# Performance work log

Hardware: AMD Instinct MI355X
Metric: run time of the kernel (lower is better)

The kernel has to match this reference:

```python
import jax, jax.numpy as jnp
import numpy as np

EMBED_DIM = 768
NUM_HEADS = 12
HEAD_DIM = EMBED_DIM // NUM_HEADS
B, N = 16, 512


def setup_inputs() -> dict:
    key = jax.random.key(0)
    ks = jax.random.split(key, 13)
    s = 1.0 / np.sqrt(EMBED_DIM)
    return {
        "query": jax.random.normal(ks[0], (B, N, EMBED_DIM), jnp.float32),
        "key_in": jax.random.normal(ks[1], (B, N, EMBED_DIM), jnp.float32),
        "value": jax.random.normal(ks[2], (B, N, EMBED_DIM), jnp.float32),
        "spatial_bias": jax.random.normal(ks[3], (B, N, N), jnp.float32),
        "edge_bias": jax.random.normal(ks[4], (B, N, N), jnp.float32),
        "Wq": jax.random.uniform(ks[5], (EMBED_DIM, EMBED_DIM), jnp.float32, -s, s),
        "bq": jax.random.uniform(ks[6], (EMBED_DIM,), jnp.float32, -s, s),
        "Wk": jax.random.uniform(ks[7], (EMBED_DIM, EMBED_DIM), jnp.float32, -s, s),
        "bk": jax.random.uniform(ks[8], (EMBED_DIM,), jnp.float32, -s, s),
        "Wv": jax.random.uniform(ks[9], (EMBED_DIM, EMBED_DIM), jnp.float32, -s, s),
        "bv": jax.random.uniform(ks[10], (EMBED_DIM,), jnp.float32, -s, s),
        "Wo": jax.random.uniform(ks[11], (EMBED_DIM, EMBED_DIM), jnp.float32, -s, s),
        "bo": jax.random.uniform(ks[12], (EMBED_DIM,), jnp.float32, -s, s),
    }


def reference(query, key_in, value, spatial_bias, edge_bias,
              Wq, bq, Wk, bk, Wv, bv, Wo, bo):
    b, n, e = query.shape
    h, d = NUM_HEADS, HEAD_DIM
    scale = d ** -0.5
    # projections (torch Linear: x @ W.T + b), reshape to [b, h, n, d]
    Q = (query @ Wq.T + bq).reshape(b, n, h, d).transpose(0, 2, 1, 3)
    K = (key_in @ Wk.T + bk).reshape(b, n, h, d).transpose(0, 2, 1, 3)
    V = (value @ Wv.T + bv).reshape(b, n, h, d).transpose(0, 2, 1, 3)
    # scores: [b, h, n, n] with additive spatial + edge bias broadcast over heads
    scores = jnp.einsum('bhnd,bhmd->bhnm', Q, K) * scale
    scores = scores + spatial_bias[:, None, :, :] + edge_bias[:, None, :, :]
    attn_weights = jax.nn.softmax(scores, axis=-1)
    attn_output = jnp.einsum('bhnm,bhmd->bhnd', attn_weights, V)
    attn_output = attn_output.transpose(0, 2, 1, 3).reshape(b, n, e)
    attn_output = attn_output @ Wo.T + bo
    return attn_output, attn_weights
```

## Files before the change

kernel.cpp:

```cpp
#include <hip/hip_runtime.h>

using bf16x8 = __attribute__((ext_vector_type(8))) __bf16;
using f32x4  = __attribute__((ext_vector_type(4))) float;
using u16 = unsigned short;

constexpr int Bb = 16, Nn = 512, Ee = 768, Hh = 12, Dd = 64;

__device__ inline u16 f2b(float x) {
  union { float f; unsigned int u; } v; v.f = x;
  unsigned int r = v.u + 0x7fffu + ((v.u >> 16) & 1u);
  return (u16)(r >> 16);
}

__device__ inline unsigned cvtpk(float lo, float hi) {
  unsigned r;
  asm("v_cvt_pk_bf16_f32 %0, %1, %2" : "=v"(r) : "v"(lo), "v"(hi));
  return r;
}

__device__ inline void gload16(const void* g, void* l) {
  __builtin_amdgcn_global_load_lds((const __attribute__((address_space(1))) void*)g,
                                   (__attribute__((address_space(3))) void*)l, 16, 0, 0);
}

#define MFMA __builtin_amdgcn_mfma_f32_16x16x32_bf16

__global__ void k_cvt(const float* __restrict__ w0, const float* __restrict__ w1,
                      const float* __restrict__ w2, const float* __restrict__ w3,
                      u16* __restrict__ dstW,
                      const float* __restrict__ sb, const float* __restrict__ eb,
                      u16* __restrict__ cb) {
  int idx = blockIdx.x * 256 + threadIdx.x;
  constexpr int perW = Ee * Ee / 4;
  constexpr int totW = 4 * perW;
  if (idx < totW) {
    int m = idx / perW, r = idx - m * perW;
    const float* src = (m == 0) ? w0 : (m == 1) ? w1 : (m == 2) ? w2 : w3;
    float4 v = reinterpret_cast<const float4*>(src)[r];
    ushort4 o = make_ushort4(f2b(v.x), f2b(v.y), f2b(v.z), f2b(v.w));
    reinterpret_cast<ushort4*>(dstW)[idx] = o;
  } else {
    int k = idx - totW;
    float4 s0 = reinterpret_cast<const float4*>(sb)[k * 2];
    float4 s1 = reinterpret_cast<const float4*>(sb)[k * 2 + 1];
    float4 e0 = reinterpret_cast<const float4*>(eb)[k * 2];
    float4 e1 = reinterpret_cast<const float4*>(eb)[k * 2 + 1];
    ushort4 o0 = make_ushort4(f2b(s0.x + e0.x), f2b(s0.y + e0.y), f2b(s0.z + e0.z), f2b(s0.w + e0.w));
    ushort4 o1 = make_ushort4(f2b(s1.x + e1.x), f2b(s1.y + e1.y), f2b(s1.z + e1.z), f2b(s1.w + e1.w));
    reinterpret_cast<ushort4*>(cb)[k * 2] = o0;
    reinterpret_cast<ushort4*>(cb)[k * 2 + 1] = o1;
  }
}

__global__ __launch_bounds__(256, 3)
void k_qkv(const float* __restrict__ xq, const float* __restrict__ xk, const float* __restrict__ xv,
           const u16* __restrict__ wb, const float* __restrict__ bq, const float* __restrict__ bk,
           const float* __restrict__ bv, u16* __restrict__ Q, u16* __restrict__ K,
           u16* __restrict__ VT) {
  const int mat = blockIdx.z;
  const float* X = (mat == 0) ? xq : (mat == 1) ? xk : xv;
  const u16* W = wb + (size_t)mat * Ee * Ee;
  const float* bias = (mat == 0) ? bq : (mat == 1) ? bk : bv;
  const int bm = blockIdx.x, bn = blockIdx.y;
  const int tid = threadIdx.x, lane = tid & 63, wid = tid >> 6;
  const int wr = wid >> 1, wc = wid & 1;

  __shared__ char smem[49152];

  auto stageA = [&](int buf, int it) {
    const int r0 = tid >> 3, s = tid & 7;
    char* lbase = smem + buf * 16384 + tid * 16;
#pragma unroll
    for (int R = 0; R < 4; ++R) {
      const int row = R * 32 + r0;
      const int ch = s ^ (row & 7);
      gload16(X + (size_t)(bm * 128 + row) * Ee + it * 32 + ch * 4, lbase + R * 4096);
    }
  };
  auto stageB = [&](int buf, int it) {
    const int r0 = tid >> 2, s = tid & 3;
    char* lbase = smem + 32768 + buf * 8192 + tid * 16;
#pragma unroll
    for (int R = 0; R < 2; ++R) {
      const int row = R * 64 + r0;
      const int ch = s ^ ((row >> 1) & 3);
      gload16(W + (size_t)(bn * 128 + row) * Ee + it * 32 + ch * 8, lbase + R * 4096);
    }
  };

  f32x4 acc[4][4] = {};

  auto compute = [&](int buf) {
    const char* Ab = smem + buf * 16384;
    const char* Bbp = smem + 32768 + buf * 8192;
    const int q = lane >> 4;
    bf16x8 a[4], b[4];
#pragma unroll
    for (int mt = 0; mt < 4; ++mt) {
      const int row = wr * 64 + mt * 16 + (lane & 15);
      const int s0 = (2 * q) ^ (row & 7), s1 = (2 * q + 1) ^ (row & 7);
      f32x4 f0 = *reinterpret_cast<const f32x4*>(Ab + row * 128 + s0 * 16);
      f32x4 f1 = *reinterpret_cast<const f32x4*>(Ab + row * 128 + s1 * 16);
      union { unsigned u[4]; bf16x8 v; } cv;
      cv.u[0] = cvtpk(f0[0], f0[1]);
      cv.u[1] = cvtpk(f0[2], f0[3]);
      cv.u[2] = cvtpk(f1[0], f1[1]);
      cv.u[3] = cvtpk(f1[2], f1[3]);
      a[mt] = cv.v;
    }
#pragma unroll
    for (int nt = 0; nt < 4; ++nt) {
      const int row = wc * 64 + nt * 16 + (lane & 15);
      const int s = q ^ ((row >> 1) & 3);
      b[nt] = *reinterpret_cast<const bf16x8*>(Bbp + row * 64 + s * 16);
    }
#pragma unroll
    for (int mt = 0; mt < 4; ++mt)
#pragma unroll
      for (int nt = 0; nt < 4; ++nt)
        acc[mt][nt] = MFMA(a[mt], b[nt], acc[mt][nt], 0, 0, 0);
  };

  stageA(0, 0); stageB(0, 0);
  __syncthreads();
  int buf = 0;
  for (int it = 0; it < 24; ++it) {
    if (it + 1 < 24) { stageA(buf ^ 1, it + 1); stageB(buf ^ 1, it + 1); }
    compute(buf);
    __syncthreads();
    buf ^= 1;
  }

  u16* sm16 = (u16*)smem;
  if (mat < 2) {
    u16* dst = (mat == 0) ? Q : K;
    const float sc = (mat == 0) ? 0.125f : 1.0f;
#pragma unroll
    for (int mt = 0; mt < 4; ++mt) {
      const int n_l0 = wr * 64 + mt * 16 + ((lane >> 4) << 2);
#pragma unroll
      for (int nt = 0; nt < 4; ++nt) {
        const int e_l = wc * 64 + nt * 16 + (lane & 15);
        const float bs = bias[bn * 128 + e_l];
#pragma unroll
        for (int j = 0; j < 4; ++j)
          sm16[(n_l0 + j) * 136 + e_l] = f2b((acc[mt][nt][j] + bs) * sc);
      }
    }
    __syncthreads();
    const int row = tid >> 1, half = tid & 1;
    const int n = bm * 128 + row, b = n >> 9, n0 = n & 511, h = bn * 2 + half;
    u16* gp = dst + ((size_t)(b * Hh + h) * Nn + n0) * Dd;
    const u16* sp = sm16 + row * 136 + half * 64;
#pragma unroll
    for (int i = 0; i < 8; ++i)
      *reinterpret_cast<int4*>(gp + i * 8) = *reinterpret_cast<const int4*>(sp + i * 8);
  } else {
#pragma unroll
    for (int mt = 0; mt < 4; ++mt) {
      const int n_l0 = wr * 64 + mt * 16 + ((lane >> 4) << 2);
#pragma unroll
      for (int nt = 0; nt < 4; ++nt) {
        const int e_l = wc * 64 + nt * 16 + (lane & 15);
        const float bs = bias[bn * 128 + e_l];
#pragma unroll
        for (int j = 0; j < 4; ++j)
          sm16[e_l * 136 + n_l0 + j] = f2b(acc[mt][nt][j] + bs);
      }
    }
    __syncthreads();
    const int er = tid >> 1, half = tid & 1;
    const int b = bm >> 2, h = bn * 2 + (er >> 6), d = er & 63;
    u16* gp = VT + ((size_t)(b * Hh + h) * Dd + d) * Nn + (bm & 3) * 128 + half * 64;
    const u16* sp = sm16 + er * 136 + half * 64;
#pragma unroll
    for (int i = 0; i < 8; ++i)
      *reinterpret_cast<int4*>(gp + i * 8) = *reinterpret_cast<const int4*>(sp + i * 8);
  }
}

__global__ __launch_bounds__(256, 2)
void k_attn(const u16* __restrict__ Q, const u16* __restrict__ K,
            const u16* __restrict__ cb, const u16* __restrict__ VT,
            float* __restrict__ wout, u16* __restrict__ AO) {
  const int flat = blockIdx.x + 8 * (blockIdx.y + Hh * blockIdx.z);
  const int c = flat & 7, j = flat >> 3;
  const int g = c + 8 * (j % 24);
  const int qb = j / 24;
  const int h = g % Hh, b = g / Hh;
  const int bh = b * Hh + h;
  const int q0 = qb * 64;
  const int tid = threadIdx.x, lane = tid & 63, wid = tid >> 6;
  const int l15 = lane & 15, q4 = lane >> 4;

  __shared__ char smem[65536];

  bf16x8 aq[2];
  {
    const u16* qp = Q + ((size_t)bh * Nn + q0 + wid * 16 + l15) * Dd + q4 * 8;
    aq[0] = *reinterpret_cast<const bf16x8*>(qp);
    aq[1] = *reinterpret_cast<const bf16x8*>(qp + 32);
  }

  const int rql = wid * 16 + l15;
  const int rq = q0 + rql;
  const u16* cbp = cb + ((size_t)b * Nn + rq) * Nn + q4 * 4;
  uint2 cbr[32];
#pragma unroll
  for (int t = 0; t < 32; ++t)
    cbr[t] = *reinterpret_cast<const uint2*>(cbp + t * 16);

#pragma unroll
  for (int i = 0; i < 16; ++i) {
    const int s = i * 256 + tid;
    const int row = s >> 3, cs = s & 7;
    gload16(K + ((size_t)bh * Nn + row) * Dd + (cs ^ (row & 7)) * 8, smem + s * 16);
  }
  __syncthreads();

  f32x4 acc[32] = {};
  __builtin_amdgcn_s_setprio(1);
#pragma unroll
  for (int kt = 0; kt < 8; ++kt)
#pragma unroll
    for (int kk = 0; kk < 2; ++kk)
#pragma unroll
      for (int ct = 0; ct < 4; ++ct) {
        const int r = kt * 64 + ct * 16 + l15;
        bf16x8 bk = *reinterpret_cast<const bf16x8*>(
            smem + r * 128 + (((kk * 4 + q4) ^ (r & 7)) * 16));
        acc[kt * 4 + ct] = MFMA(bk, aq[kk], acc[kt * 4 + ct], 0, 0, 0);
      }
  __builtin_amdgcn_s_setprio(0);

#pragma unroll
  for (int t = 0; t < 32; ++t) {
    acc[t][0] += __uint_as_float((unsigned)cbr[t].x << 16);
    acc[t][1] += __uint_as_float(cbr[t].x & 0xffff0000u);
    acc[t][2] += __uint_as_float((unsigned)cbr[t].y << 16);
    acc[t][3] += __uint_as_float(cbr[t].y & 0xffff0000u);
  }

  float mx = -1e30f;
#pragma unroll
  for (int t = 0; t < 32; ++t)
#pragma unroll
    for (int j2 = 0; j2 < 4; ++j2) mx = fmaxf(mx, acc[t][j2]);
  mx = fmaxf(mx, __shfl_xor(mx, 16));
  mx = fmaxf(mx, __shfl_xor(mx, 32));

  float sum = 0.f;
#pragma unroll
  for (int t = 0; t < 32; ++t)
#pragma unroll
    for (int j2 = 0; j2 < 4; ++j2) {
      float p = exp2f((acc[t][j2] - mx) * 1.44269504f);
      acc[t][j2] = p;
      sum += p;
    }
  sum += __shfl_xor(sum, 16);
  sum += __shfl_xor(sum, 32);
  const float inv = 1.0f / sum;

  __syncthreads();

  const u16* Vb = VT + ((size_t)bh * Dd + l15) * Nn + q4 * 8;
  bf16x8 vb0[8], vb1[8];
  auto loadV = [&](int kt, bf16x8* d) {
#pragma unroll
    for (int kk = 0; kk < 2; ++kk)
#pragma unroll
      for (int ct = 0; ct < 4; ++ct)
        d[kk * 4 + ct] = *reinterpret_cast<const bf16x8*>(
            Vb + (size_t)(ct * 16) * Nn + kt * 64 + kk * 32);
  };
  loadV(0, vb0);
  loadV(1, vb1);

  char* Pb = smem + rql * 1024;
#pragma unroll
  for (int t = 0; t < 32; ++t) {
    uint2 pk;
    pk.x = cvtpk(acc[t][0] * inv, acc[t][1] * inv);
    pk.y = cvtpk(acc[t][2] * inv, acc[t][3] * inv);
    const int chunk = (2 * t + (q4 >> 1)) ^ (rql & 7);
    *reinterpret_cast<uint2*>(Pb + chunk * 16 + (q4 & 1) * 8) = pk;
  }
  __syncthreads();

  f32x4 acc2[4] = {};
  const int qr = rql;
  const char* Pr = smem + qr * 1024;
  f32x4* wp4 = reinterpret_cast<f32x4*>(wout + ((size_t)bh * Nn + rq) * Nn);
  auto storeW = [&](int kt) {
#pragma unroll
    for (int u = 0; u < 4; ++u) {
      const int t = kt * 4 + u;
      f32x4 o;
      o[0] = acc[t][0] * inv; o[1] = acc[t][1] * inv;
      o[2] = acc[t][2] * inv; o[3] = acc[t][3] * inv;
      __builtin_nontemporal_store(o, &wp4[t * 4 + q4]);
    }
  };
#pragma unroll
  for (int kp = 0; kp < 4; ++kp) {
    const int ktA = 2 * kp, ktB = 2 * kp + 1;
    __builtin_amdgcn_s_setprio(1);
#pragma unroll
    for (int kk = 0; kk < 2; ++kk) {
      const int chunk = (ktA * 8 + kk * 4 + q4) ^ (qr & 7);
      bf16x8 pa = *reinterpret_cast<const bf16x8*>(Pr + chunk * 16);
#pragma unroll
      for (int ct = 0; ct < 4; ++ct)
        acc2[ct] = MFMA(pa, vb0[kk * 4 + ct], acc2[ct], 0, 0, 0);
    }
    __builtin_amdgcn_s_setprio(0);
    if (ktA + 2 < 8) loadV(ktA + 2, vb0);
    storeW(ktA);
    __builtin_amdgcn_s_setprio(1);
#pragma unroll
    for (int kk = 0; kk < 2; ++kk) {
      const int chunk = (ktB * 8 + kk * 4 + q4) ^ (qr & 7);
      bf16x8 pa = *reinterpret_cast<const bf16x8*>(Pr + chunk * 16);
#pragma unroll
      for (int ct = 0; ct < 4; ++ct)
        acc2[ct] = MFMA(pa, vb1[kk * 4 + ct], acc2[ct], 0, 0, 0);
    }
    __builtin_amdgcn_s_setprio(0);
    if (ktB + 2 < 8) loadV(ktB + 2, vb1);
    storeW(ktB);
  }

  __syncthreads();
  u16* ao_t = (u16*)smem;
#pragma unroll
  for (int ct = 0; ct < 4; ++ct)
#pragma unroll
    for (int j2 = 0; j2 < 4; ++j2)
      ao_t[(wid * 16 + q4 * 4 + j2) * 72 + ct * 16 + l15] = f2b(acc2[ct][j2]);
  __syncthreads();
  {
    const int row = tid >> 3, ch = tid & 7;
#pragma unroll
    for (int i = 0; i < 2; ++i) {
      const int r = row + i * 32;
      int4 v = *reinterpret_cast<const int4*>(ao_t + r * 72 + ch * 8);
      *reinterpret_cast<int4*>(AO + ((size_t)b * Nn + q0 + r) * Ee + h * Dd + ch * 8) = v;
    }
  }
}

__global__ __launch_bounds__(256, 4)
void k_outproj(const u16* __restrict__ AOp, const u16* __restrict__ Wo,
               const float* __restrict__ bo, float* __restrict__ out) {
  const int bm = blockIdx.x, bn = blockIdx.y;
  const int tid = threadIdx.x, lane = tid & 63, wid = tid >> 6;
  const int wr = wid >> 1, wc = wid & 1;

  __shared__ char smem[32768];

  auto stage = [&](const u16* src, int lds_base, int buf, int it) {
    const int r0 = tid >> 2, s = tid & 3;
    char* lbase = smem + lds_base + buf * 8192 + tid * 16;
#pragma unroll
    for (int R = 0; R < 2; ++R) {
      const int row = R * 64 + r0;
      const int ch = s ^ ((row >> 1) & 3);
      gload16(src + (size_t)row * Ee + it * 32 + ch * 8, lbase + R * 4096);
    }
  };

  f32x4 acc[4][4] = {};

  auto compute = [&](int buf) {
    const char* Ab = smem + buf * 8192;
    const char* Bbp = smem + 16384 + buf * 8192;
    const int q = lane >> 4;
    bf16x8 a[4], b[4];
#pragma unroll
    for (int mt = 0; mt < 4; ++mt) {
      const int row = wr * 64 + mt * 16 + (lane & 15);
      const int s = q ^ ((row >> 1) & 3);
      a[mt] = *reinterpret_cast<const bf16x8*>(Ab + row * 64 + s * 16);
    }
#pragma unroll
    for (int nt = 0; nt < 4; ++nt) {
      const int row = wc * 64 + nt * 16 + (lane & 15);
      const int s = q ^ ((row >> 1) & 3);
      b[nt] = *reinterpret_cast<const bf16x8*>(Bbp + row * 64 + s * 16);
    }
#pragma unroll
    for (int mt = 0; mt < 4; ++mt)
#pragma unroll
      for (int nt = 0; nt < 4; ++nt)
        acc[mt][nt] = MFMA(a[mt], b[nt], acc[mt][nt], 0, 0, 0);
  };

  const u16* Asrc = AOp + (size_t)(bm * 128) * Ee;
  const u16* Bsrc = Wo + (size_t)(bn * 128) * Ee;
  stage(Asrc, 0, 0, 0); stage(Bsrc, 16384, 0, 0);
  __syncthreads();
  int buf = 0;
  for (int it = 0; it < 24; ++it) {
    if (it + 1 < 24) { stage(Asrc, 0, buf ^ 1, it + 1); stage(Bsrc, 16384, buf ^ 1, it + 1); }
    compute(buf);
    __syncthreads();
    buf ^= 1;
  }

#pragma unroll
  for (int mt = 0; mt < 4; ++mt) {
#pragma unroll
    for (int nt = 0; nt < 4; ++nt) {
      const int ecol = bn * 128 + wc * 64 + nt * 16 + (lane & 15);
      const int r0 = bm * 128 + wr * 64 + mt * 16 + ((lane >> 4) << 2);
      const float bs = bo[ecol];
      f32x4 v = acc[mt][nt];
#pragma unroll
      for (int j = 0; j < 4; ++j)
        __builtin_nontemporal_store(v[j] + bs, &out[(size_t)(r0 + j) * Ee + ecol]);
    }
  }
}

extern "C" void kernel_launch(void* const* d_in, const int* in_sizes, int n_in,
                              void* d_out, int out_size, void* d_ws, size_t ws_size,
                              hipStream_t stream) {
  const float* query  = (const float*)d_in[0];
  const float* key_in = (const float*)d_in[1];
  const float* value  = (const float*)d_in[2];
  const float* sb     = (const float*)d_in[3];
  const float* eb     = (const float*)d_in[4];
  const float* Wq     = (const float*)d_in[5];
  const float* bq     = (const float*)d_in[6];
  const float* Wk     = (const float*)d_in[7];
  const float* bk     = (const float*)d_in[8];
  const float* Wv     = (const float*)d_in[9];
  const float* bv     = (const float*)d_in[10];
  const float* Wo     = (const float*)d_in[11];
  const float* bo     = (const float*)d_in[12];

  float* out0 = (float*)d_out;
  float* wout = out0 + (size_t)Bb * Nn * Ee;

  char* ws = (char*)d_ws;
  const size_t off_wb = 0;
  const size_t off_Q  = 4718592;
  const size_t off_K  = 17301504;
  const size_t off_VT = 29884416;
  const size_t off_AO = 42467328;
  const size_t off_cb = 55050240;
  if (ws_size < 63438848) return;

  u16* wb  = (u16*)(ws + off_wb);
  u16* Qs  = (u16*)(ws + off_Q);
  u16* Kst = (u16*)(ws + off_K);
  u16* VTs = (u16*)(ws + off_VT);
  u16* AO  = (u16*)(ws + off_AO);
  u16* cbf = (u16*)(ws + off_cb);

  k_cvt<<<4352, 256, 0, stream>>>(Wq, Wk, Wv, Wo, wb, sb, eb, cbf);
  k_qkv<<<dim3(64, 6, 3), 256, 0, stream>>>(query, key_in, value, wb, bq, bk, bv, Qs, Kst, VTs);
  k_attn<<<dim3(8, Hh, Bb), 256, 0, stream>>>(Qs, Kst, cbf, VTs, wout, AO);
  k_outproj<<<dim3(64, 6), 256, 0, stream>>>(AO, wb + 3 * Ee * Ee, bo, out0);
}
```

Baseline: 175.3 us.

## Split K tile load to overlap second half with first-half QK MFMAs

The K tile load into shared memory is split into two halves. The MFMAs for the first half are issued while the second half's async loads are still in flight, with a barrier between the halves. The normalized probabilities are now written back into acc once and reused for both the bf16 P pack and the fp32 weight store, which removes duplicate multiplies. The attention-output staging gets its own shared buffer so a final barrier can be dropped, at the cost of about 9KB more LDS per block, which may reduce occupancy.

```diff
diff --git a/kernel.cpp b/kernel.cpp
--- a/kernel.cpp
+++ b/kernel.cpp
@@ -194,6 +194,7 @@
   const int l15 = lane & 15, q4 = lane >> 4;
 
   __shared__ char smem[65536];
+  __shared__ u16 ao_t[64 * 72];
 
   bf16x8 aq[2];
   {
@@ -211,17 +212,24 @@
     cbr[t] = *reinterpret_cast<const uint2*>(cbp + t * 16);
 
 #pragma unroll
-  for (int i = 0; i < 16; ++i) {
+  for (int i = 0; i < 8; ++i) {
     const int s = i * 256 + tid;
     const int row = s >> 3, cs = s & 7;
     gload16(K + ((size_t)bh * Nn + row) * Dd + (cs ^ (row & 7)) * 8, smem + s * 16);
   }
   __syncthreads();
 
+#pragma unroll
+  for (int i = 8; i < 16; ++i) {
+    const int s = i * 256 + tid;
+    const int row = s >> 3, cs = s & 7;
+    gload16(K + ((size_t)bh * Nn + row) * Dd + (cs ^ (row & 7)) * 8, smem + s * 16);
+  }
+
   f32x4 acc[32] = {};
   __builtin_amdgcn_s_setprio(1);
 #pragma unroll
-  for (int kt = 0; kt < 8; ++kt)
+  for (int kt = 0; kt < 4; ++kt)
 #pragma unroll
     for (int kk = 0; kk < 2; ++kk)
 #pragma unroll
@@ -232,6 +240,21 @@
         acc[kt * 4 + ct] = MFMA(bk, aq[kk], acc[kt * 4 + ct], 0, 0, 0);
       }
   __builtin_amdgcn_s_setprio(0);
+  __syncthreads();
+
+  __builtin_amdgcn_s_setprio(1);
+#pragma unroll
+  for (int kt = 4; kt < 8; ++kt)
+#pragma unroll
+    for (int kk = 0; kk < 2; ++kk)
+#pragma unroll
+      for (int ct = 0; ct < 4; ++ct) {
+        const int r = kt * 64 + ct * 16 + l15;
+        bf16x8 bk = *reinterpret_cast<const bf16x8*>(
+            smem + r * 128 + (((kk * 4 + q4) ^ (r & 7)) * 16));
+        acc[kt * 4 + ct] = MFMA(bk, aq[kk], acc[kt * 4 + ct], 0, 0, 0);
+      }
+  __builtin_amdgcn_s_setprio(0);
 
 #pragma unroll
   for (int t = 0; t < 32; ++t) {
@@ -280,9 +303,10 @@
   char* Pb = smem + rql * 1024;
 #pragma unroll
   for (int t = 0; t < 32; ++t) {
+    acc[t][0] *= inv; acc[t][1] *= inv; acc[t][2] *= inv; acc[t][3] *= inv;
     uint2 pk;
-    pk.x = cvtpk(acc[t][0] * inv, acc[t][1] * inv);
-    pk.y = cvtpk(acc[t][2] * inv, acc[t][3] * inv);
+    pk.x = cvtpk(acc[t][0], acc[t][1]);
+    pk.y = cvtpk(acc[t][2], acc[t][3]);
     const int chunk = (2 * t + (q4 >> 1)) ^ (rql & 7);
     *reinterpret_cast<uint2*>(Pb + chunk * 16 + (q4 & 1) * 8) = pk;
   }
@@ -296,10 +320,7 @@
 #pragma unroll
     for (int u = 0; u < 4; ++u) {
       const int t = kt * 4 + u;
-      f32x4 o;
-      o[0] = acc[t][0] * inv; o[1] = acc[t][1] * inv;
-      o[2] = acc[t][2] * inv; o[3] = acc[t][3] * inv;
-      __builtin_nontemporal_store(o, &wp4[t * 4 + q4]);
+      __builtin_nontemporal_store(acc[t], &wp4[t * 4 + q4]);
     }
   };
 #pragma unroll
@@ -331,8 +352,6 @@
     storeW(ktB);
   }
 
-  __syncthreads();
-  u16* ao_t = (u16*)smem;
 #pragma unroll
   for (int ct = 0; ct < 4; ++ct)
 #pragma unroll
```

Result: no change. 176.3 us (+0.6%).
